# Optimization experiments

Measured on AMD Instinct MI355X. Metric: run time of the kernel, lower is better.

## Reference

```python
import jax, jax.numpy as jnp
import numpy as np

B = 2048
NUM_FIELDS = 32
EMBED = 64
P = NUM_FIELDS * (NUM_FIELDS - 1) // 2  # 496 field pairs

# Pair indices (i < j), identical to the row_idx/col_idx loops in __init__
_ROW, _COL = np.triu_indices(NUM_FIELDS, k=1)
ROW_IDX = jnp.asarray(_ROW, dtype=jnp.int32)
COL_IDX = jnp.asarray(_COL, dtype=jnp.int32)


def setup_inputs() -> dict:
    key = jax.random.key(0)
    k1, k2 = jax.random.split(key)
    emb_inputs = jax.random.normal(k1, (B, NUM_FIELDS, EMBED), dtype=jnp.float32)
    # kernel_type='mat' -> kernel shape (E, P, E), xavier_normal-like init
    fan_in = P * EMBED
    fan_out = EMBED
    std = float(np.sqrt(2.0 / (fan_in + fan_out)))
    kernel = jax.random.normal(k2, (EMBED, P, EMBED), dtype=jnp.float32) * std
    return {"emb_inputs": emb_inputs, "kernel": kernel}


def reference(emb_inputs, kernel):
    # Gather field pairs: p, q shape (B, P, E)
    p = emb_inputs[:, ROW_IDX]
    q = emb_inputs[:, COL_IDX]
    # torch named-tensor chain for kernel_type='mat':
    #   kp[b, h, n] = sum_e p[b, n, e] * kernel[h, n, e]
    #   out[b, n]   = sum_h kp[b, h, n] * q[b, n, h]
    # Fused: out[b, n] = sum_{e, h} p[b, n, e] * kernel[h, n, e] * q[b, n, h]
    return jnp.einsum('bne,hne,bnh->bn', p, kernel, q)
```

## Files before the change

### kernel.cpp

```cpp
#include <hip/hip_runtime.h>


#define B_TOT 2048
#define NF    32
#define EMB   64
#define NP    496
#define BT    32

typedef short bf16x8 __attribute__((ext_vector_type(8)));
typedef short bf16x4 __attribute__((ext_vector_type(4)));
typedef float f32x4  __attribute__((ext_vector_type(4)));

static __device__ inline unsigned f2bf(float f) {
    unsigned u = __builtin_bit_cast(unsigned, f);
    u += 0x7fffu + ((u >> 16) & 1u);
    return u >> 16;
}
static __device__ inline unsigned pack2(float lo, float hi) {
    return f2bf(lo) | (f2bf(hi) << 16);
}
static __device__ inline float bf2f(short s) {
    return __builtin_bit_cast(float, (unsigned)((unsigned short)s) << 16);
}

#define AS1 __attribute__((address_space(1)))
#define AS3 __attribute__((address_space(3)))

__global__ __launch_bounds__(256) void prep(const float* __restrict__ kern,
                                            const float* __restrict__ emb,
                                            short* __restrict__ kb,
                                            short* __restrict__ ebf) {
    __shared__ short w[EMB * 72];
    if (blockIdx.x < NP) {
        const int n = blockIdx.x;
#pragma unroll
        for (int j = 0; j < 4; ++j) {
            const int idx = threadIdx.x + 256 * j;
            const int h = idx >> 4, e4 = idx & 15;
            const f32x4 v = *(const f32x4*)(kern + ((size_t)h * NP + n) * EMB + e4 * 4);
            uint2 u;
            u.x = pack2(v[0], v[1]);
            u.y = pack2(v[2], v[3]);
            *(uint2*)&w[h * 72 + e4 * 4] = u;
        }
        __syncthreads();
#pragma unroll
        for (int j = 0; j < 2; ++j) {
            const int u    = threadIdx.x + 256 * j;
            const int frag = u >> 6, l = u & 63;
            const int h  = (frag >> 1) * 16 + (l & 15);
            const int e0 = (frag & 1) * 32 + (l >> 4) * 8;
            const bf16x8 t = *(const bf16x8*)&w[h * 72 + e0];
            *(bf16x8*)(kb + (size_t)n * 4096 + u * 8) = t;
        }
    } else {
        const int t    = (blockIdx.x - NP) * 256 + threadIdx.x;
        const int cidx = t & 127;
        const int f    = (t >> 7) & 31;
        const int bt16 = t >> 12;
        const int bp = cidx >> 3, x = cidx & 7;
        const int ec = x ^ (bp & 7);
        const float* src = emb + (((size_t)(bt16 * 16 + bp) * NF + f) * EMB + ec * 8);
        const f32x4 a = *(const f32x4*)src;
        const f32x4 b = *(const f32x4*)(src + 4);
        uint4 u;
        u.x = pack2(a[0], a[1]); u.y = pack2(a[2], a[3]);
        u.z = pack2(b[0], b[1]); u.w = pack2(b[2], b[3]);
        *(uint4*)(ebf + (size_t)t * 8) = u;
    }
}

__global__ __launch_bounds__(512, 4) void opnl_main(
    const short* __restrict__ ebf,
    const short* __restrict__ kb,
    float* __restrict__ out)
{
    __shared__ short elds[16 * 2 * 1024];

    const int type = blockIdx.x >> 6;
    const int bt   = blockIdx.x & 63;
    const int b0   = bt * BT;

    int bLo, bHi, npr;
    switch (type) {
        case 0: case 1: bLo = 0;  bHi = 0;  npr = 60; break;
        case 2: case 3: bLo = 16; bHi = 16; npr = 60; break;
        case 4:         bLo = 0;  bHi = 8;  npr = 64; break;
        case 5:         bLo = 8;  bHi = 16; npr = 64; break;
        case 6:         bLo = 0;  bHi = 16; npr = 64; break;
        default:        bLo = 8;  bHi = 8;  npr = 64; break;
    }

    const int lane = threadIdx.x & 63;
    const int wid  = threadIdx.x >> 6;
    const int lo4  = lane & 15;
    const int hi4  = lane >> 4;

#pragma unroll
    for (int i = 0; i < 4; ++i) {
        const int s   = wid * 4 + i;
        const int lf  = s >> 1, sub = s & 1;
        const int gf  = lf + (lf < 8 ? bLo : bHi);
        const short* src = ebf + ((size_t)((bt * 2 + sub) * 32 + gf)) * 1024;
        __builtin_amdgcn_global_load_lds((const AS1 void*)(src + lane * 8),
                                         (AS3 void*)&elds[s * 1024], 16, 0, 0);
        __builtin_amdgcn_global_load_lds((const AS1 void*)(src + 512 + lane * 8),
                                         (AS3 void*)&elds[s * 1024 + 512], 16, 0, 0);
    }
    __syncthreads();

    auto pairK = [&](int k, int& lr, int& lc, int& nn) {
        int pr = wid + 8 * k;
        if (pr >= npr) pr -= npr;
        if (type < 4) {
            int pig = (type & 1) * 60 + pr;
            int r = 0;
            while (pig >= 15 - r) { pig -= 15 - r; ++r; }
            lr = r; lc = r + 1 + pig;
        } else {
            lr = pr >> 3; lc = 8 + (pr & 7);
        }
        const int R = lr + (lr < 8 ? bLo : bHi);
        const int C = lc + (lc < 8 ? bLo : bHi);
        nn = R * (63 - R) / 2 + (C - R - 1);
    };

    auto loadW = [&](bf16x8 (&wf)[4][2], int nn) {
        const bf16x8* wp = (const bf16x8*)(kb + (size_t)nn * 4096);
#pragma unroll
        for (int mh = 0; mh < 4; ++mh)
#pragma unroll
            for (int kc = 0; kc < 2; ++kc)
                wf[mh][kc] = wp[(mh * 2 + kc) * 64 + lane];
    };

    auto compute = [&](bf16x8 (&wf)[4][2], int lr, int lc, int nn) {
#pragma unroll
        for (int sub = 0; sub < 2; ++sub) {
            const int bb = sub * 16 + lo4;

            bf16x8 pf[2];
#pragma unroll
            for (int kc = 0; kc < 2; ++kc)
                pf[kc] = *(const bf16x8*)
                    &elds[(lr * 2 + sub) * 1024 +
                          (lo4 * 8 + (((kc * 4 + hi4) ^ (lo4 & 7)))) * 8];

            f32x4 acc[4] = {f32x4{0,0,0,0}, f32x4{0,0,0,0},
                            f32x4{0,0,0,0}, f32x4{0,0,0,0}};
#pragma unroll
            for (int mh = 0; mh < 4; ++mh)
#pragma unroll
                for (int kc = 0; kc < 2; ++kc)
                    acc[mh] = __builtin_amdgcn_mfma_f32_16x16x32_bf16(
                        wf[mh][kc], pf[kc], acc[mh], 0, 0, 0);

            float val = 0.f;
#pragma unroll
            for (int mh = 0; mh < 4; ++mh) {
                const bf16x4 q = *(const bf16x4*)
                    &elds[(lc * 2 + sub) * 1024 +
                          (lo4 * 8 + (((mh * 2 + (hi4 >> 1)) ^ (lo4 & 7)))) * 8 +
                          (hi4 & 1) * 4];
                val += acc[mh][0] * bf2f(q[0]) + acc[mh][1] * bf2f(q[1])
                     + acc[mh][2] * bf2f(q[2]) + acc[mh][3] * bf2f(q[3]);
            }
            val += __shfl_xor(val, 16, 64);
            val += __shfl_xor(val, 32, 64);
            if (lane < 16) out[(size_t)(b0 + bb) * NP + nn] = val;
        }
    };

    bf16x8 wA[4][2], wB[4][2];
    int lrA, lcA, nA, lrB, lcB, nB;
    pairK(0, lrA, lcA, nA);
    loadW(wA, nA);
#pragma unroll
    for (int k = 0; k < 8; ++k) {
        if ((k & 1) == 0) {
            if (k < 7) { pairK(k + 1, lrB, lcB, nB); loadW(wB, nB); }
            compute(wA, lrA, lcA, nA);
        } else {
            if (k < 7) { pairK(k + 1, lrA, lcA, nA); loadW(wA, nA); }
            compute(wB, lrB, lcB, nB);
        }
    }
}

extern "C" void kernel_launch(void* const* d_in, const int* in_sizes, int n_in,
                              void* d_out, int out_size, void* d_ws, size_t ws_size,
                              hipStream_t stream) {
    const float* emb  = (const float*)d_in[0];
    const float* kern = (const float*)d_in[1];
    float*       out  = (float*)d_out;

    short* kb  = (short*)d_ws;
    short* ebf = (short*)((char*)d_ws + (4 << 20));

    prep<<<NP + (B_TOT * NF * EMB / 8) / 256, 256, 0, stream>>>(kern, emb, kb, ebf);
    opnl_main<<<8 * 64, 512, 0, stream>>>(ebf, kb, out);
}
```

Baseline: 29.17 us.

## Switch to 32x32x16 MFMA with 64-row batch tiles and 1024-thread blocks

Replaces the 16x16x32 bf16 MFMA tiling with 32x32x16 MFMAs, repacks the kernel weights in prep to match the new fragment layout, and doubles the batch tile to 64 rows per block using 1024-thread blocks and 128KB of LDS. The runtime while-loop that decodes pair indices becomes a constant lookup table. The double-buffered weight prefetch across pairs is dropped. The aim is fewer, larger MFMAs and more reuse of each weight load across batch rows, at the cost of only 256 blocks, one block per CU because of the LDS size, and no explicit load/compute overlap.

```diff
diff --git a/kernel.cpp b/kernel.cpp
--- a/kernel.cpp
+++ b/kernel.cpp
@@ -5,11 +5,12 @@
 #define NF    32
 #define EMB   64
 #define NP    496
-#define BT    32
+#define BT    64
 
 typedef short bf16x8 __attribute__((ext_vector_type(8)));
 typedef short bf16x4 __attribute__((ext_vector_type(4)));
 typedef float f32x4  __attribute__((ext_vector_type(4)));
+typedef float f32x16 __attribute__((ext_vector_type(16)));
 
 static __device__ inline unsigned f2bf(float f) {
     unsigned u = __builtin_bit_cast(unsigned, f);
@@ -25,6 +26,24 @@
 
 #define AS1 __attribute__((address_space(1)))
 #define AS3 __attribute__((address_space(3)))
+
+__device__ const unsigned char PAIR_T16[120] = {
+    0x01,0x02,0x03,0x04,0x05,0x06,0x07,0x08,0x09,0x0A,0x0B,0x0C,0x0D,0x0E,0x0F,
+    0x12,0x13,0x14,0x15,0x16,0x17,0x18,0x19,0x1A,0x1B,0x1C,0x1D,0x1E,0x1F,
+    0x23,0x24,0x25,0x26,0x27,0x28,0x29,0x2A,0x2B,0x2C,0x2D,0x2E,0x2F,
+    0x34,0x35,0x36,0x37,0x38,0x39,0x3A,0x3B,0x3C,0x3D,0x3E,0x3F,
+    0x45,0x46,0x47,0x48,0x49,0x4A,0x4B,0x4C,0x4D,0x4E,0x4F,
+    0x56,0x57,0x58,0x59,0x5A,0x5B,0x5C,0x5D,0x5E,0x5F,
+    0x67,0x68,0x69,0x6A,0x6B,0x6C,0x6D,0x6E,0x6F,
+    0x78,0x79,0x7A,0x7B,0x7C,0x7D,0x7E,0x7F,
+    0x89,0x8A,0x8B,0x8C,0x8D,0x8E,0x8F,
+    0x9A,0x9B,0x9C,0x9D,0x9E,0x9F,
+    0xAB,0xAC,0xAD,0xAE,0xAF,
+    0xBC,0xBD,0xBE,0xBF,
+    0xCD,0xCE,0xCF,
+    0xDE,0xDF,
+    0xEF
+};
 
 __global__ __launch_bounds__(256) void prep(const float* __restrict__ kern,
                                             const float* __restrict__ emb,
@@ -48,8 +67,8 @@
         for (int j = 0; j < 2; ++j) {
             const int u    = threadIdx.x + 256 * j;
             const int frag = u >> 6, l = u & 63;
-            const int h  = (frag >> 1) * 16 + (l & 15);
-            const int e0 = (frag & 1) * 32 + (l >> 4) * 8;
+            const int h  = (frag >> 2) * 32 + (l & 31);
+            const int e0 = (frag & 3) * 16 + (l >> 5) * 8;
             const bf16x8 t = *(const bf16x8*)&w[h * 72 + e0];
             *(bf16x8*)(kb + (size_t)n * 4096 + u * 8) = t;
         }
@@ -70,15 +89,15 @@
     }
 }
 
-__global__ __launch_bounds__(512, 4) void opnl_main(
+__global__ __launch_bounds__(1024) void opnl_main(
     const short* __restrict__ ebf,
     const short* __restrict__ kb,
     float* __restrict__ out)
 {
-    __shared__ short elds[16 * 2 * 1024];
-
-    const int type = blockIdx.x >> 6;
-    const int bt   = blockIdx.x & 63;
+    __shared__ short elds[64 * 1024];
+
+    const int type = blockIdx.x >> 5;
+    const int bt   = blockIdx.x & 31;
     const int b0   = bt * BT;
 
     int bLo, bHi, npr;
@@ -93,15 +112,16 @@
 
     const int lane = threadIdx.x & 63;
     const int wid  = threadIdx.x >> 6;
-    const int lo4  = lane & 15;
-    const int hi4  = lane >> 4;
+    const int bp   = lane & 15;
+    const int l5   = lane >> 5;
+    const int sub_lo = (lane >> 4) & 1;
 
 #pragma unroll
     for (int i = 0; i < 4; ++i) {
-        const int s   = wid * 4 + i;
-        const int lf  = s >> 1, sub = s & 1;
-        const int gf  = lf + (lf < 8 ? bLo : bHi);
-        const short* src = ebf + ((size_t)((bt * 2 + sub) * 32 + gf)) * 1024;
+        const int s     = wid * 4 + i;
+        const int lf    = s >> 2, sub16 = s & 3;
+        const int gf    = lf + (lf < 8 ? bLo : bHi);
+        const short* src = ebf + ((size_t)((bt * 4 + sub16) * 32 + gf)) * 1024;
         __builtin_amdgcn_global_load_lds((const AS1 void*)(src + lane * 8),
                                          (AS3 void*)&elds[s * 1024], 16, 0, 0);
         __builtin_amdgcn_global_load_lds((const AS1 void*)(src + 512 + lane * 8),
@@ -109,80 +129,67 @@
     }
     __syncthreads();
 
-    auto pairK = [&](int k, int& lr, int& lc, int& nn) {
-        int pr = wid + 8 * k;
+    for (int k = 0; k < 4; ++k) {
+        int pr = wid + 16 * k;
         if (pr >= npr) pr -= npr;
+        int lr, lc;
         if (type < 4) {
-            int pig = (type & 1) * 60 + pr;
-            int r = 0;
-            while (pig >= 15 - r) { pig -= 15 - r; ++r; }
-            lr = r; lc = r + 1 + pig;
+            const int pig = __builtin_amdgcn_readfirstlane((type & 1) * 60 + pr);
+            const int byt = PAIR_T16[pig];
+            lr = byt >> 4; lc = byt & 15;
         } else {
             lr = pr >> 3; lc = 8 + (pr & 7);
         }
-        const int R = lr + (lr < 8 ? bLo : bHi);
-        const int C = lc + (lc < 8 ? bLo : bHi);
-        nn = R * (63 - R) / 2 + (C - R - 1);
-    };
-
-    auto loadW = [&](bf16x8 (&wf)[4][2], int nn) {
+        const int R  = lr + (lr < 8 ? bLo : bHi);
+        const int C  = lc + (lc < 8 ? bLo : bHi);
+        const int nn = R * (63 - R) / 2 + (C - R - 1);
+
+        bf16x8 wf[2][4];
         const bf16x8* wp = (const bf16x8*)(kb + (size_t)nn * 4096);
 #pragma unroll
-        for (int mh = 0; mh < 4; ++mh)
-#pragma unroll
-            for (int kc = 0; kc < 2; ++kc)
-                wf[mh][kc] = wp[(mh * 2 + kc) * 64 + lane];
-    };
-
-    auto compute = [&](bf16x8 (&wf)[4][2], int lr, int lc, int nn) {
-#pragma unroll
-        for (int sub = 0; sub < 2; ++sub) {
-            const int bb = sub * 16 + lo4;
-
-            bf16x8 pf[2];
-#pragma unroll
-            for (int kc = 0; kc < 2; ++kc)
-                pf[kc] = *(const bf16x8*)
-                    &elds[(lr * 2 + sub) * 1024 +
-                          (lo4 * 8 + (((kc * 4 + hi4) ^ (lo4 & 7)))) * 8];
-
-            f32x4 acc[4] = {f32x4{0,0,0,0}, f32x4{0,0,0,0},
-                            f32x4{0,0,0,0}, f32x4{0,0,0,0}};
-#pragma unroll
-            for (int mh = 0; mh < 4; ++mh)
-#pragma unroll
-                for (int kc = 0; kc < 2; ++kc)
-                    acc[mh] = __builtin_amdgcn_mfma_f32_16x16x32_bf16(
-                        wf[mh][kc], pf[kc], acc[mh], 0, 0, 0);
+        for (int mt = 0; mt < 2; ++mt)
+#pragma unroll
+            for (int ks = 0; ks < 4; ++ks)
+                wf[mt][ks] = wp[(mt * 4 + ks) * 64 + lane];
+
+#pragma unroll
+        for (int hb = 0; hb < 2; ++hb) {
+            const int sub16 = hb * 2 + sub_lo;
+            const int segp  = (lr * 4 + sub16) * 1024;
+            const int segq  = (lc * 4 + sub16) * 1024;
+
+            bf16x8 pf[4];
+#pragma unroll
+            for (int ks = 0; ks < 4; ++ks) {
+                const int ec = ks * 2 + l5;
+                pf[ks] = *(const bf16x8*)&elds[segp + (bp * 8 + (ec ^ (bp & 7))) * 8];
+            }
+
+            f32x16 acc[2] = {
+                f32x16{0,0,0,0,0,0,0,0,0,0,0,0,0,0,0,0},
+                f32x16{0,0,0,0,0,0,0,0,0,0,0,0,0,0,0,0}};
+#pragma unroll
+            for (int ks = 0; ks < 4; ++ks) {
+                acc[0] = __builtin_amdgcn_mfma_f32_32x32x16_bf16(
+                    wf[0][ks], pf[ks], acc[0], 0, 0, 0);
+                acc[1] = __builtin_amdgcn_mfma_f32_32x32x16_bf16(
+                    wf[1][ks], pf[ks], acc[1], 0, 0, 0);
+            }
 
             float val = 0.f;
 #pragma unroll
-            for (int mh = 0; mh < 4; ++mh) {
-                const bf16x4 q = *(const bf16x4*)
-                    &elds[(lc * 2 + sub) * 1024 +
-                          (lo4 * 8 + (((mh * 2 + (hi4 >> 1)) ^ (lo4 & 7)))) * 8 +
-                          (hi4 & 1) * 4];
-                val += acc[mh][0] * bf2f(q[0]) + acc[mh][1] * bf2f(q[1])
-                     + acc[mh][2] * bf2f(q[2]) + acc[mh][3] * bf2f(q[3]);
+            for (int mt = 0; mt < 2; ++mt) {
+#pragma unroll
+                for (int rg2 = 0; rg2 < 4; ++rg2) {
+                    const bf16x4 qv = *(const bf16x4*)
+                        &elds[segq + (bp * 8 + ((mt * 4 + rg2) ^ (bp & 7))) * 8 + l5 * 4];
+#pragma unroll
+                    for (int i = 0; i < 4; ++i)
+                        val = fmaf(acc[mt][rg2 * 4 + i], bf2f(qv[i]), val);
+                }
             }
-            val += __shfl_xor(val, 16, 64);
             val += __shfl_xor(val, 32, 64);
-            if (lane < 16) out[(size_t)(b0 + bb) * NP + nn] = val;
-        }
-    };
-
-    bf16x8 wA[4][2], wB[4][2];
-    int lrA, lcA, nA, lrB, lcB, nB;
-    pairK(0, lrA, lcA, nA);
-    loadW(wA, nA);
-#pragma unroll
-    for (int k = 0; k < 8; ++k) {
-        if ((k & 1) == 0) {
-            if (k < 7) { pairK(k + 1, lrB, lcB, nB); loadW(wB, nB); }
-            compute(wA, lrA, lcA, nA);
-        } else {
-            if (k < 7) { pairK(k + 1, lrA, lcA, nA); loadW(wA, nA); }
-            compute(wB, lrB, lcB, nB);
+            if (lane < 32) out[(size_t)(b0 + hb * 32 + lane) * NP + nn] = val;
         }
     }
 }
@@ -198,5 +205,5 @@
     short* ebf = (short*)((char*)d_ws + (4 << 20));
 
     prep<<<NP + (B_TOT * NF * EMB / 8) / 256, 256, 0, stream>>>(kern, emb, kb, ebf);
-    opnl_main<<<8 * 64, 512, 0, stream>>>(ebf, kb, out);
-}
+    opnl_main<<<8 * 32, 1024, 0, stream>>>(ebf, kb, out);
+}
```

Result: no change. 29.31 us (+0.5%).
